# Kernel optimization log

Hardware: AMD Instinct MI355X
Metric: run time of the kernel (lower is better)

## Reference

```python
import jax, jax.numpy as jnp
import numpy as np

K_PLG = 9
LN_EPS = 1e-5

def _layer_norm(x, g, b):
    mu = jnp.mean(x, axis=-1, keepdims=True)
    v = jnp.mean((x - mu) ** 2, axis=-1, keepdims=True)
    return (x - mu) / jnp.sqrt(v + LN_EPS) * g + b

def _label_to_patch_agg(label, patch, k):
    # squared euclidean distances (S, N); sqrt is monotonic so top-k indices
    # match torch.cdist(p=2).topk(largest=False)
    d2 = (jnp.sum(label * label, axis=1)[:, None]
          + jnp.sum(patch * patch, axis=1)[None, :]
          - 2.0 * label @ patch.T)
    _, idx = jax.lax.top_k(-d2, k)          # (S, k) nearest
    nbr = patch[idx]                         # (S, k, C)
    return jnp.max(nbr - label[:, None, :], axis=1)  # max-relative diff (S, C)

def setup_inputs() -> dict:
    key = jax.random.key(0)
    ks = jax.random.split(key, 12)
    N, C = 100000, 256
    n_mood, n_genre, n_sub = 64, 256, 1024
    s = 1.0 / np.sqrt(C)
    return {
        "patch_emb": jax.random.normal(ks[0], (N, C), jnp.float32),
        "mood_emb": jax.random.normal(ks[1], (n_mood, C), jnp.float32),
        "genre_emb": jax.random.normal(ks[2], (n_genre, C), jnp.float32),
        "sub_emb": jax.random.normal(ks[3], (n_sub, C), jnp.float32),
        "Wm": jax.random.normal(ks[4], (2 * C, C), jnp.float32) * s,
        "bm": jnp.zeros((C,), jnp.float32),
        "Wg": jax.random.normal(ks[5], (3 * C, C), jnp.float32) * s,
        "bg": jnp.zeros((C,), jnp.float32),
        "Ws": jax.random.normal(ks[6], (4 * C, C), jnp.float32) * s,
        "bs": jnp.zeros((C,), jnp.float32),
        "gm": jnp.ones((C,), jnp.float32), "bnm": jnp.zeros((C,), jnp.float32),
        "gg": jnp.ones((C,), jnp.float32), "bng": jnp.zeros((C,), jnp.float32),
        "gs": jnp.ones((C,), jnp.float32), "bns": jnp.zeros((C,), jnp.float32),
    }

def reference(patch_emb, mood_emb, genre_emb, sub_emb,
              Wm, bm, Wg, bg, Ws, bs, gm, bnm, gg, bng, gs, bns):
    k = K_PLG
    # mood level
    ctx_m = _label_to_patch_agg(mood_emb, patch_emb, k)
    mood = _layer_norm(
        mood_emb + jnp.concatenate([mood_emb, ctx_m], axis=-1) @ Wm + bm, gm, bnm)
    # genre level
    ctx_g_p = _label_to_patch_agg(genre_emb, patch_emb, k)
    ctx_g_m = _label_to_patch_agg(genre_emb, mood, max(1, k // 2))
    genre = _layer_norm(
        genre_emb + jnp.concatenate([genre_emb, ctx_g_p, ctx_g_m], axis=-1) @ Wg + bg,
        gg, bng)
    # sub-genre level
    ctx_s_p = _label_to_patch_agg(sub_emb, patch_emb, k)
    ctx_s_m = _label_to_patch_agg(sub_emb, mood, max(1, k // 3))
    ctx_s_g = _label_to_patch_agg(sub_emb, genre, max(1, k // 2))
    sub = _layer_norm(
        sub_emb + jnp.concatenate([sub_emb, ctx_s_p, ctx_s_m, ctx_s_g], axis=-1) @ Ws + bs,
        gs, bns)
    return (mood, genre, sub)
```

## Files before the change

kernel.cpp:

```cpp
#include <hip/hip_runtime.h>
#include <float.h>

#define N_PATCH 100000
#define C 256
#define S_TOT 1344
#define LBLK 32
#define NGRP 42
#define NCHUNK 24
#define CHUNKP 4224
#define NTILE 1563
#define KCC 10
#define NCAND (NCHUNK*KCC)
#define NSEL 24
#define KP 9
#define SMASK 0xFFFFE000u
#define KINIT 0x7F7FFFFFu

typedef __attribute__((ext_vector_type(4))) float f32x4;
typedef __attribute__((ext_vector_type(2))) long i64x2;
typedef __attribute__((ext_vector_type(4))) unsigned int u32x4;

static __device__ __forceinline__ unsigned int pk4_fp8(float a, float b, float c, float d) {
  int v = __builtin_amdgcn_cvt_pk_fp8_f32(a, b, 0, false);
  v = __builtin_amdgcn_cvt_pk_fp8_f32(c, d, v, true);
  return (unsigned int)v;
}

#define KNET3(K0, K1, K2, KV)                               \
  { unsigned int _kv = (KV);                                \
    K2 = min(K2, max(K1, _kv));                             \
    K1 = min(K1, max(K0, _kv));                             \
    K0 = min(K0, _kv); }

__global__ __launch_bounds__(256) void k_prep(
    const float* __restrict__ patch, const float* __restrict__ me,
    const float* __restrict__ ge, const float* __restrict__ se,
    unsigned char* __restrict__ patchT, unsigned char* __restrict__ lblQ,
    float* __restrict__ hp2) {
  __shared__ float4 xs[4096];
  int bid = blockIdx.x;
  int t = threadIdx.x;
  if (bid < NTILE) {
    const int T = bid;
    const int w = t >> 6, l = t & 63;
    #pragma unroll
    for (int i = 0; i < 16; ++i) {
      int row = 4 * i + w;
      int grow = min(T * 64 + row, N_PATCH - 1);
      float4 v = reinterpret_cast<const float4*>(patch + (size_t)grow * C)[l];
      xs[row * 64 + (l ^ (row & 7))] = v;
      float s = v.x*v.x + v.y*v.y + v.z*v.z + v.w*v.w;
      #pragma unroll
      for (int off = 32; off; off >>= 1) s += __shfl_down(s, off, 64);
      if (l == 0 && T * 64 + row < N_PATCH) hp2[T * 64 + row] = 0.5f * s + 512.0f;
    }
    __syncthreads();
    const int q = (t >> 6) & 3, g = (t >> 4) & 3, r16 = t & 15;
    const int b4 = 16 * q + 2 * g;
    #pragma unroll
    for (int u = 0; u < 4; ++u) {
      int rr = u * 16 + r16;
      int xm = rr & 7;
      float4 aa = xs[rr * 64 + ((b4    ) ^ xm)];
      float4 bb = xs[rr * 64 + ((b4 + 1) ^ xm)];
      float4 cc = xs[rr * 64 + ((b4 + 8) ^ xm)];
      float4 dd = xs[rr * 64 + ((b4 + 9) ^ xm)];
      u32x4 o;
      o.x = pk4_fp8(-aa.x, -aa.y, -aa.z, -aa.w);
      o.y = pk4_fp8(-bb.x, -bb.y, -bb.z, -bb.w);
      o.z = pk4_fp8(-cc.x, -cc.y, -cc.z, -cc.w);
      o.w = pk4_fp8(-dd.x, -dd.y, -dd.z, -dd.w);
      *reinterpret_cast<u32x4*>(patchT + ((size_t)T << 14) + (size_t)(u * 256 + t) * 16) = o;
    }
  } else {
    int row = (bid - NTILE) * 4 + (t >> 6);
    int l = t & 63;
    int k0 = 32 * ((l >> 1) & 7) + 8 * (l >> 4) + (l & 1) * 4;
    const float* src = (row < 64) ? me + (size_t)row * C
                     : (row < 320) ? ge + (size_t)(row - 64) * C
                                   : se + (size_t)(row - 320) * C;
    float4 v = *reinterpret_cast<const float4*>(src + k0);
    *reinterpret_cast<unsigned int*>(lblQ + (size_t)row * 256 + l * 4) =
        pk4_fp8(v.x, v.y, v.z, v.w);
  }
}

__global__ __launch_bounds__(256, 4) void k_score_mfma(
    const unsigned char* __restrict__ patchT, const unsigned char* __restrict__ lblQ,
    const float* __restrict__ hp2,
    float* __restrict__ candS, int* __restrict__ candI) {
  __shared__ unsigned int ksmem[LBLK * 48];

  const int j = blockIdx.x;
  const int chunk = (j & 7) * 3 + (j >> 3) / NGRP;
  const int grp = (j >> 3) % NGRP;
  const int row0 = grp * LBLK;
  const int p_begin = chunk * CHUNKP;
  const int p_end = min(p_begin + CHUNKP, N_PATCH);
  const int tid = threadIdx.x;
  const int l = tid & 63, w = tid >> 6;
  const int g = l >> 4, r16 = l & 15;

  long bf0[8], bf1[8];
  {
    const unsigned char* b0 = lblQ + ((size_t)(row0 + r16) << 8) + (g << 6);
    #pragma unroll
    for (int q = 0; q < 4; ++q) {
      i64x2 v0 = *reinterpret_cast<const i64x2*>(b0 + q * 16);
      i64x2 v1 = *reinterpret_cast<const i64x2*>(b0 + 4096 + q * 16);
      bf0[2*q] = v0.x; bf0[2*q+1] = v0.y;
      bf1[2*q] = v1.x; bf1[2*q+1] = v1.y;
    }
  }

  unsigned int a0k = KINIT, a1k = KINIT, a2k = KINIT;
  unsigned int b0k = KINIT, b1k = KINIT, b2k = KINIT;

  const int nsteps = (p_end - p_begin + 63) >> 6;
  const int gtile0 = p_begin >> 6;
  const unsigned char* pbase = patchT + ((size_t)gtile0 << 14) + (w << 12) + (l << 4);
  const int hsub = w * 16 + 4 * g;

  i64x2 A0[4], A1[4];
  float4 h0, h1;

  auto loadA = [&](int t, i64x2 (&A)[4]) {
    const unsigned char* p = pbase + ((size_t)t << 14);
    #pragma unroll
    for (int q = 0; q < 4; ++q) A[q] = *reinterpret_cast<const i64x2*>(p + (q << 10));
  };
  auto loadH = [&](int t) -> float4 {
    int hi = p_begin + t * 64 + hsub;
    if (hi > N_PATCH - 4) hi = N_PATCH - 4;
    return *reinterpret_cast<const float4*>(hp2 + hi);
  };

  auto compute = [&](i64x2 (&A)[4], float4 h, int t) {
    f32x4 acc0 = {h.x, h.y, h.z, h.w};
    f32x4 acc1 = acc0;
    __builtin_amdgcn_s_setprio(1);
    #pragma unroll
    for (int q = 0; q < 4; ++q) {
      acc0 = __builtin_amdgcn_mfma_f32_16x16x32_fp8_fp8(A[q].x, bf0[2*q],   acc0, 0, 0, 0);
      acc1 = __builtin_amdgcn_mfma_f32_16x16x32_fp8_fp8(A[q].x, bf1[2*q],   acc1, 0, 0, 0);
      acc0 = __builtin_amdgcn_mfma_f32_16x16x32_fp8_fp8(A[q].y, bf0[2*q+1], acc0, 0, 0, 0);
      acc1 = __builtin_amdgcn_mfma_f32_16x16x32_fp8_fp8(A[q].y, bf1[2*q+1], acc1, 0, 0, 0);
    }
    __builtin_amdgcn_s_setprio(0);
    unsigned int lidx = (unsigned int)(t * 64 + hsub);
    unsigned int l1 = lidx | 1u, l2 = lidx | 2u, l3 = lidx | 3u;
    if (p_begin + t * 64 + 64 <= p_end) {
      KNET3(a0k, a1k, a2k, (__float_as_uint(acc0[0]) & SMASK) | lidx);
      KNET3(a0k, a1k, a2k, (__float_as_uint(acc0[1]) & SMASK) | l1);
      KNET3(a0k, a1k, a2k, (__float_as_uint(acc0[2]) & SMASK) | l2);
      KNET3(a0k, a1k, a2k, (__float_as_uint(acc0[3]) & SMASK) | l3);
      KNET3(b0k, b1k, b2k, (__float_as_uint(acc1[0]) & SMASK) | lidx);
      KNET3(b0k, b1k, b2k, (__float_as_uint(acc1[1]) & SMASK) | l1);
      KNET3(b0k, b1k, b2k, (__float_as_uint(acc1[2]) & SMASK) | l2);
      KNET3(b0k, b1k, b2k, (__float_as_uint(acc1[3]) & SMASK) | l3);
    } else {
      const int pg0 = p_begin + t * 64 + hsub;
      unsigned int k0 = (pg0     < p_end) ? ((__float_as_uint(acc0[0]) & SMASK) | lidx) : KINIT;
      unsigned int k1 = (pg0 + 1 < p_end) ? ((__float_as_uint(acc0[1]) & SMASK) | l1) : KINIT;
      unsigned int k2 = (pg0 + 2 < p_end) ? ((__float_as_uint(acc0[2]) & SMASK) | l2) : KINIT;
      unsigned int k3 = (pg0 + 3 < p_end) ? ((__float_as_uint(acc0[3]) & SMASK) | l3) : KINIT;
      unsigned int m0 = (pg0     < p_end) ? ((__float_as_uint(acc1[0]) & SMASK) | lidx) : KINIT;
      unsigned int m1 = (pg0 + 1 < p_end) ? ((__float_as_uint(acc1[1]) & SMASK) | l1) : KINIT;
      unsigned int m2 = (pg0 + 2 < p_end) ? ((__float_as_uint(acc1[2]) & SMASK) | l2) : KINIT;
      unsigned int m3 = (pg0 + 3 < p_end) ? ((__float_as_uint(acc1[3]) & SMASK) | l3) : KINIT;
      KNET3(a0k, a1k, a2k, k0); KNET3(a0k, a1k, a2k, k1);
      KNET3(a0k, a1k, a2k, k2); KNET3(a0k, a1k, a2k, k3);
      KNET3(b0k, b1k, b2k, m0); KNET3(b0k, b1k, b2k, m1);
      KNET3(b0k, b1k, b2k, m2); KNET3(b0k, b1k, b2k, m3);
    }
  };

  loadA(0, A0); h0 = loadH(0);
  for (int t = 0; t < nsteps; t += 2) {
    loadA(t + 1, A1); h1 = loadH(t + 1);
    compute(A0, h0, t);
    loadA(t + 2, A0); h0 = loadH(t + 2);
    if (t + 1 < nsteps) compute(A1, h1, t + 1);
  }
  __syncthreads();

  const int sub = (w << 2) + g;
  {
    int base0 = (r16 * 16 + sub) * 3;
    int base1 = ((r16 + 16) * 16 + sub) * 3;
    ksmem[base0 + 0] = a0k; ksmem[base0 + 1] = a1k; ksmem[base0 + 2] = a2k;
    ksmem[base1 + 0] = b0k; ksmem[base1 + 1] = b1k; ksmem[base1 + 2] = b2k;
  }
  __syncthreads();
  if (tid < LBLK) {
    unsigned int fk[KCC];
    #pragma unroll
    for (int jj = 0; jj < KCC; ++jj) fk[jj] = KINIT;
    for (int q = 0; q < 48; ++q) {
      unsigned int v = ksmem[tid * 48 + q];
      if (v < fk[KCC-1]) {
        fk[KCC-1] = v;
        #pragma unroll
        for (int qq = KCC-1; qq >= 1; --qq) {
          if (fk[qq] < fk[qq-1]) {
            unsigned int tv = fk[qq]; fk[qq] = fk[qq-1]; fk[qq-1] = tv;
          }
        }
      }
    }
    size_t o = ((size_t)(row0 + tid) * NCHUNK + chunk) * KCC;
    #pragma unroll
    for (int jj = 0; jj < KCC; ++jj) {
      candS[o + jj] = __uint_as_float(fk[jj] & SMASK);
      candI[o + jj] = p_begin + (int)(fk[jj] & 0x1FFFu);
    }
  }
}

__global__ __launch_bounds__(256) void k_rescore_ctx(
    const float* __restrict__ patchF,
    const float* __restrict__ me, const float* __restrict__ ge,
    const float* __restrict__ se,
    const float* __restrict__ hp2, const float* __restrict__ candS,
    const int* __restrict__ candI,
    float* __restrict__ ctx_m, float* __restrict__ ctx_gp, float* __restrict__ ctx_sp,
    const float* __restrict__ Wm, const float* __restrict__ bm,
    const float* __restrict__ gm, const float* __restrict__ bnm,
    float* __restrict__ out_m) {
  __shared__ float lrow[C];
  __shared__ float crow[C];
  __shared__ float ss[NCAND];
  __shared__ int si[NCAND];
  __shared__ int selIdx[NSEL];
  __shared__ float s2[NSEL];
  __shared__ int top[KP];
  __shared__ float red2[4];
  int row = blockIdx.x, t = threadIdx.x;
  const float* lsrc = (row < 64) ? me + (size_t)row * C
                    : (row < 320) ? ge + (size_t)(row - 64) * C
                                  : se + (size_t)(row - 320) * C;
  lrow[t] = lsrc[t];
  if (t < NCAND) {
    ss[t] = candS[(size_t)row * NCAND + t];
    si[t] = candI[(size_t)row * NCAND + t];
  }
  __syncthreads();
  if (t < NCAND) {
    float s = ss[t]; int id = si[t];
    int rank = 0;
    for (int q = 0; q < NCAND; ++q) {
      float v = ss[q];
      rank += (v < s) || (v == s && si[q] < id);
    }
    if (rank < NSEL) selIdx[rank] = id;
  }
  __syncthreads();
  {
    int c = t >> 3, l8 = t & 7;
    if (c < NSEL) {
      const float4* pr = reinterpret_cast<const float4*>(patchF + (size_t)selIdx[c] * C);
      const float4* lr = reinterpret_cast<const float4*>(lrow);
      float dx = 0.f, dy = 0.f, dz = 0.f, dw = 0.f;
      #pragma unroll
      for (int i = 0; i < 8; ++i) {
        float4 a = pr[l8 + 8*i], b = lr[l8 + 8*i];
        dx = fmaf(a.x, b.x, dx); dy = fmaf(a.y, b.y, dy);
        dz = fmaf(a.z, b.z, dz); dw = fmaf(a.w, b.w, dw);
      }
      float d = (dx + dy) + (dz + dw);
      #pragma unroll
      for (int off = 1; off < 8; off <<= 1) d += __shfl_xor(d, off, 64);
      if (l8 == 0) s2[c] = hp2[selIdx[c]] - d;
    }
  }
  __syncthreads();
  if (t == 0) {
    float fs[KP]; int fi[KP];
    #pragma unroll
    for (int jj = 0; jj < KP; ++jj) { fs[jj] = FLT_MAX; fi[jj] = 0; }
    for (int q = 0; q < NSEL; ++q) {
      float v = s2[q];
      if (v < fs[KP-1]) {
        fs[KP-1] = v; fi[KP-1] = selIdx[q];
        #pragma unroll
        for (int qq = KP-1; qq >= 1; --qq) {
          if (fs[qq] < fs[qq-1]) {
            float ts = fs[qq]; fs[qq] = fs[qq-1]; fs[qq-1] = ts;
            int ti = fi[qq]; fi[qq] = fi[qq-1]; fi[qq-1] = ti;
          }
        }
      }
    }
    #pragma unroll
    for (int jj = 0; jj < KP; ++jj) top[jj] = fi[jj];
  }
  __syncthreads();
  float m = -FLT_MAX;
  #pragma unroll
  for (int jj = 0; jj < KP; ++jj)
    m = fmaxf(m, patchF[(size_t)top[jj] * C + t]);
  float ctxv = m - lrow[t];
  float* dst; int rr;
  if (row < 64)       { dst = ctx_m;  rr = row; }
  else if (row < 320) { dst = ctx_gp; rr = row - 64; }
  else                { dst = ctx_sp; rr = row - 320; }
  dst[(size_t)rr * C + t] = ctxv;
  if (row < 64) {
    crow[t] = ctxv;
    __syncthreads();
    float acc = 0.f;
    for (int i0 = 0; i0 < 256; i0 += 16) {
      float wv[16];
      #pragma unroll
      for (int u = 0; u < 16; ++u) wv[u] = Wm[(size_t)(i0 + u) * C + t];
      #pragma unroll
      for (int u = 0; u < 16; ++u) acc = fmaf(lrow[i0 + u], wv[u], acc);
    }
    for (int i0 = 0; i0 < 256; i0 += 16) {
      float wv[16];
      #pragma unroll
      for (int u = 0; u < 16; ++u) wv[u] = Wm[(size_t)(256 + i0 + u) * C + t];
      #pragma unroll
      for (int u = 0; u < 16; ++u) acc = fmaf(crow[i0 + u], wv[u], acc);
    }
    float y = lrow[t] + acc + bm[t];
    int w = t >> 6, ln = t & 63;
    float sum = y;
    #pragma unroll
    for (int off = 32; off; off >>= 1) sum += __shfl_down(sum, off, 64);
    if (ln == 0) red2[w] = sum;
    __syncthreads();
    float mu = (red2[0] + red2[1] + red2[2] + red2[3]) * (1.f / C);
    __syncthreads();
    float d = y - mu;
    float sq = d * d;
    #pragma unroll
    for (int off = 32; off; off >>= 1) sq += __shfl_down(sq, off, 64);
    if (ln == 0) red2[w] = sq;
    __syncthreads();
    float var = (red2[0] + red2[1] + red2[2] + red2[3]) * (1.f / C);
    out_m[(size_t)row * C + t] = d * rsqrtf(var + 1e-5f) * gm[t] + bnm[t];
  }
}

__global__ __launch_bounds__(512) void k_out_g(
    const float* __restrict__ genre_e, const float* __restrict__ ctx_gp,
    const float* __restrict__ out_m,
    const float* __restrict__ W, const float* __restrict__ bias,
    const float* __restrict__ gamma, const float* __restrict__ beta,
    float* __restrict__ out) {
  __shared__ float x[2][1024];
  __shared__ float ds[2][64];
  __shared__ int sel[2][4];
  __shared__ float part[2][2][256];
  __shared__ float red[4][2];
  const int row0 = blockIdx.x * 2, t = threadIdx.x;
  const int w = t >> 6, ln = t & 63;
  if (t < 256) {
    int rr = t >> 7, seg = (t >> 6) & 1, c4 = (t & 63) << 2;
    const float* src = seg ? ctx_gp : genre_e;
    *reinterpret_cast<float4*>(&x[rr][seg * 256 + c4]) =
        *reinterpret_cast<const float4*>(src + (size_t)(row0 + rr) * C + c4);
  }
  __syncthreads();
  {
    int q = t & 3, pr = t >> 2;
    int rr = pr >> 6, ri = pr & 63;
    const float4* rp = reinterpret_cast<const float4*>(out_m + (size_t)ri * C);
    const float4* qp = reinterpret_cast<const float4*>(x[rr]);
    float s = 0.f;
    #pragma unroll
    for (int i = 0; i < 16; ++i) {
      float4 a = rp[i * 4 + q];
      float4 b = qp[i * 4 + q];
      float e;
      e = a.x - b.x; s = fmaf(e, e, s); e = a.y - b.y; s = fmaf(e, e, s);
      e = a.z - b.z; s = fmaf(e, e, s); e = a.w - b.w; s = fmaf(e, e, s);
    }
    s += __shfl_xor(s, 1, 64);
    s += __shfl_xor(s, 2, 64);
    if (q == 0) ds[rr][ri] = s;
  }
  __syncthreads();
  if (w < 2) {
    for (int jj = 0; jj < 4; ++jj) {
      float m = ds[w][ln]; int mi_ = ln;
      #pragma unroll
      for (int off = 32; off; off >>= 1) {
        float om = __shfl_down(m, off, 64);
        int oi = __shfl_down(mi_, off, 64);
        if (om < m) { m = om; mi_ = oi; }
      }
      mi_ = __shfl(mi_, 0, 64);
      if (ln == 0) sel[w][jj] = mi_;
      ds[w][mi_] = FLT_MAX;
    }
  }
  __syncthreads();
  {
    int rr = t >> 8, c = t & 255;
    float m = -FLT_MAX;
    #pragma unroll
    for (int jj = 0; jj < 4; ++jj) m = fmaxf(m, out_m[(size_t)sel[rr][jj] * C + c]);
    x[rr][512 + c] = m - x[rr][c];
  }
  __syncthreads();
  const int kg = t >> 8, col = t & 255, base = kg * 384;
  float a0 = 0.f, a1 = 0.f;
  for (int i0 = 0; i0 < 384; i0 += 16) {
    float wv[16];
    #pragma unroll
    for (int u = 0; u < 16; ++u) wv[u] = W[(size_t)(base + i0 + u) * C + col];
    #pragma unroll
    for (int u = 0; u < 16; ++u) {
      a0 = fmaf(x[0][base + i0 + u], wv[u], a0);
      a1 = fmaf(x[1][base + i0 + u], wv[u], a1);
    }
  }
  part[kg][0][col] = a0; part[kg][1][col] = a1;
  __syncthreads();
  if (t < 256) {
    float bv = bias[t];
    float y0 = x[0][t] + part[0][0][t] + part[1][0][t] + bv;
    float y1 = x[1][t] + part[0][1][t] + part[1][1][t] + bv;
    float s0 = y0, s1 = y1;
    #pragma unroll
    for (int off = 32; off; off >>= 1) {
      s0 += __shfl_down(s0, off, 64);
      s1 += __shfl_down(s1, off, 64);
    }
    if (ln == 0) { red[w][0] = s0; red[w][1] = s1; }
    __syncthreads();
    float mu0 = (red[0][0] + red[1][0] + red[2][0] + red[3][0]) * (1.f / C);
    float mu1 = (red[0][1] + red[1][1] + red[2][1] + red[3][1]) * (1.f / C);
    __syncthreads();
    float d0 = y0 - mu0, d1 = y1 - mu1;
    s0 = d0 * d0; s1 = d1 * d1;
    #pragma unroll
    for (int off = 32; off; off >>= 1) {
      s0 += __shfl_down(s0, off, 64);
      s1 += __shfl_down(s1, off, 64);
    }
    if (ln == 0) { red[w][0] = s0; red[w][1] = s1; }
    __syncthreads();
    float v0 = (red[0][0] + red[1][0] + red[2][0] + red[3][0]) * (1.f / C);
    float v1 = (red[0][1] + red[1][1] + red[2][1] + red[3][1]) * (1.f / C);
    float gv = gamma[t], bbv = beta[t];
    out[(size_t)(row0    ) * C + t] = d0 * rsqrtf(v0 + 1e-5f) * gv + bbv;
    out[(size_t)(row0 + 1) * C + t] = d1 * rsqrtf(v1 + 1e-5f) * gv + bbv;
  }
}

__global__ __launch_bounds__(512) void k_out_s(
    const float* __restrict__ sub_e, const float* __restrict__ ctx_sp,
    const float* __restrict__ out_m, const float* __restrict__ out_g,
    const float* __restrict__ W, const float* __restrict__ bias,
    const float* __restrict__ gamma, const float* __restrict__ beta,
    float* __restrict__ out) {
  __shared__ float x[4][1024];
  __shared__ float ds[4][256];
  __shared__ int sel[4][4];
  __shared__ float part[2][4][256];
  __shared__ float red[4][4];
  const int row0 = blockIdx.x * 4, t = threadIdx.x;
  const int w = t >> 6, ln = t & 63;
  {
    int rr = t >> 7, seg = (t >> 6) & 1, c4 = (t & 63) << 2;
    const float* src = seg ? ctx_sp : sub_e;
    *reinterpret_cast<float4*>(&x[rr][seg * 256 + c4]) =
        *reinterpret_cast<const float4*>(src + (size_t)(row0 + rr) * C + c4);
  }
  __syncthreads();
  #pragma unroll
  for (int u = 0; u < 2; ++u) {
    int unit = u * 512 + t;
    int q = unit & 3, pr = unit >> 2;
    int rr = pr >> 6, ri = pr & 63;
    const float4* rp = reinterpret_cast<const float4*>(out_m + (size_t)ri * C);
    const float4* qp = reinterpret_cast<const float4*>(x[rr]);
    float s = 0.f;
    #pragma unroll
    for (int i = 0; i < 16; ++i) {
      float4 a = rp[i * 4 + q];
      float4 b = qp[i * 4 + q];
      float e;
      e = a.x - b.x; s = fmaf(e, e, s); e = a.y - b.y; s = fmaf(e, e, s);
      e = a.z - b.z; s = fmaf(e, e, s); e = a.w - b.w; s = fmaf(e, e, s);
    }
    s += __shfl_xor(s, 1, 64);
    s += __shfl_xor(s, 2, 64);
    if (q == 0) ds[rr][ri] = s;
  }
  __syncthreads();
  if (w < 4) {
    for (int jj = 0; jj < 3; ++jj) {
      float m = ds[w][ln]; int mi_ = ln;
      #pragma unroll
      for (int off = 32; off; off >>= 1) {
        float om = __shfl_down(m, off, 64);
        int oi = __shfl_down(mi_, off, 64);
        if (om < m) { m = om; mi_ = oi; }
      }
      mi_ = __shfl(mi_, 0, 64);
      if (ln == 0) sel[w][jj] = mi_;
      ds[w][mi_] = FLT_MAX;
    }
  }
  __syncthreads();
  #pragma unroll
  for (int u = 0; u < 2; ++u) {
    int idx = u * 512 + t;
    int rr = idx >> 8, c = idx & 255;
    float m = -FLT_MAX;
    #pragma unroll
    for (int jj = 0; jj < 3; ++jj) m = fmaxf(m, out_m[(size_t)sel[rr][jj] * C + c]);
    x[rr][512 + c] = m - x[rr][c];
  }
  __syncthreads();
  #pragma unroll
  for (int u = 0; u < 8; ++u) {
    int unit = u * 512 + t;
    int q = unit & 3, pr = unit >> 2;
    int rr = pr >> 8, ri = pr & 255;
    const float4* rp = reinterpret_cast<const float4*>(out_g + (size_t)ri * C);
    const float4* qp = reinterpret_cast<const float4*>(x[rr]);
    float s = 0.f;
    #pragma unroll
    for (int i = 0; i < 16; ++i) {
      float4 a = rp[i * 4 + q];
      float4 b = qp[i * 4 + q];
      float e;
      e = a.x - b.x; s = fmaf(e, e, s); e = a.y - b.y; s = fmaf(e, e, s);
      e = a.z - b.z; s = fmaf(e, e, s); e = a.w - b.w; s = fmaf(e, e, s);
    }
    s += __shfl_xor(s, 1, 64);
    s += __shfl_xor(s, 2, 64);
    if (q == 0) ds[rr][ri] = s;
  }
  __syncthreads();
  if (w < 4) {
    for (int jj = 0; jj < 4; ++jj) {
      float m = ds[w][ln]; int mi_ = ln;
      #pragma unroll
      for (int o = 64; o < 256; o += 64) {
        float v = ds[w][ln + o];
        if (v < m) { m = v; mi_ = ln + o; }
      }
      #pragma unroll
      for (int off = 32; off; off >>= 1) {
        float om = __shfl_down(m, off, 64);
        int oi = __shfl_down(mi_, off, 64);
        if (om < m) { m = om; mi_ = oi; }
      }
      mi_ = __shfl(mi_, 0, 64);
      if (ln == 0) sel[w][jj] = mi_;
      ds[w][mi_] = FLT_MAX;
    }
  }
  __syncthreads();
  #pragma unroll
  for (int u = 0; u < 2; ++u) {
    int idx = u * 512 + t;
    int rr = idx >> 8, c = idx & 255;
    float m = -FLT_MAX;
    #pragma unroll
    for (int jj = 0; jj < 4; ++jj) m = fmaxf(m, out_g[(size_t)sel[rr][jj] * C + c]);
    x[rr][768 + c] = m - x[rr][c];
  }
  __syncthreads();
  const int kg = t >> 8, col = t & 255, base = kg * 512;
  float acc[4] = {0.f, 0.f, 0.f, 0.f};
  for (int i0 = 0; i0 < 512; i0 += 16) {
    float wv[16];
    #pragma unroll
    for (int u = 0; u < 16; ++u) wv[u] = W[(size_t)(base + i0 + u) * C + col];
    #pragma unroll
    for (int u = 0; u < 16; ++u) {
      #pragma unroll
      for (int rr = 0; rr < 4; ++rr) acc[rr] = fmaf(x[rr][base + i0 + u], wv[u], acc[rr]);
    }
  }
  #pragma unroll
  for (int rr = 0; rr < 4; ++rr) part[kg][rr][col] = acc[rr];
  __syncthreads();
  if (t < 256) {
    float bv = bias[t];
    float y[4], d[4];
    #pragma unroll
    for (int rr = 0; rr < 4; ++rr) {
      y[rr] = x[rr][t] + part[0][rr][t] + part[1][rr][t] + bv;
      float sum = y[rr];
      #pragma unroll
      for (int off = 32; off; off >>= 1) sum += __shfl_down(sum, off, 64);
      if (ln == 0) red[w][rr] = sum;
    }
    __syncthreads();
    float mu[4];
    #pragma unroll
    for (int rr = 0; rr < 4; ++rr)
      mu[rr] = (red[0][rr] + red[1][rr] + red[2][rr] + red[3][rr]) * (1.f / C);
    __syncthreads();
    #pragma unroll
    for (int rr = 0; rr < 4; ++rr) {
      d[rr] = y[rr] - mu[rr];
      float sq = d[rr] * d[rr];
      #pragma unroll
      for (int off = 32; off; off >>= 1) sq += __shfl_down(sq, off, 64);
      if (ln == 0) red[w][rr] = sq;
    }
    __syncthreads();
    #pragma unroll
    for (int rr = 0; rr < 4; ++rr) {
      float var = (red[0][rr] + red[1][rr] + red[2][rr] + red[3][rr]) * (1.f / C);
      out[(size_t)(row0 + rr) * C + t] = d[rr] * rsqrtf(var + 1e-5f) * gamma[t] + beta[t];
    }
  }
}

extern "C" void kernel_launch(void* const* d_in, const int* in_sizes, int n_in,
                              void* d_out, int out_size, void* d_ws, size_t ws_size,
                              hipStream_t stream) {
  const float* patch   = (const float*)d_in[0];
  const float* mood_e  = (const float*)d_in[1];
  const float* genre_e = (const float*)d_in[2];
  const float* sub_e   = (const float*)d_in[3];
  const float* Wm  = (const float*)d_in[4];
  const float* bm  = (const float*)d_in[5];
  const float* Wg  = (const float*)d_in[6];
  const float* bg  = (const float*)d_in[7];
  const float* Ws  = (const float*)d_in[8];
  const float* bs_ = (const float*)d_in[9];
  const float* gm  = (const float*)d_in[10];
  const float* bnm = (const float*)d_in[11];
  const float* gg  = (const float*)d_in[12];
  const float* bng = (const float*)d_in[13];
  const float* gs  = (const float*)d_in[14];
  const float* bns = (const float*)d_in[15];

  char* ws = (char*)d_ws;
  size_t off = 0;
  auto alloc = [&](size_t bytes) { void* p = ws + off; off = (off + bytes + 255) & ~(size_t)255; return p; };
  unsigned char* patchT = (unsigned char*)alloc((size_t)(NTILE + 2) * 16384);
  unsigned char* lblQ   = (unsigned char*)alloc((size_t)S_TOT * 256);
  float* hp2   = (float*)alloc((size_t)N_PATCH * 4);
  float* candS = (float*)alloc((size_t)S_TOT * NCAND * 4);
  int*   candI = (int*)  alloc((size_t)S_TOT * NCAND * 4);
  float* ctx_m  = (float*)alloc((size_t)64   * C * 4);
  float* ctx_gp = (float*)alloc((size_t)256  * C * 4);
  float* ctx_sp = (float*)alloc((size_t)1024 * C * 4);

  float* out_m = (float*)d_out;
  float* out_g = out_m + 64 * C;
  float* out_s = out_g + 256 * C;

  k_prep<<<NTILE + S_TOT / 4, 256, 0, stream>>>(patch, mood_e, genre_e, sub_e,
                                                patchT, lblQ, hp2);
  k_score_mfma<<<NGRP * NCHUNK, 256, 0, stream>>>(patchT, lblQ, hp2, candS, candI);
  k_rescore_ctx<<<S_TOT, 256, 0, stream>>>(patch, mood_e, genre_e, sub_e, hp2,
                                           candS, candI, ctx_m, ctx_gp, ctx_sp,
                                           Wm, bm, gm, bnm, out_m);
  k_out_g<<<128, 512, 0, stream>>>(genre_e, ctx_gp, out_m, Wg, bg, gg, bng, out_g);
  k_out_s<<<256, 512, 0, stream>>>(sub_e, ctx_sp, out_m, out_g, Ws, bs_, gs, bns, out_s);
}
```

Before: 186.4 us.

## Merge two label groups per score block so waves share patch tile loads

The scoring kernel now uses 512-thread blocks covering 64 labels instead of 256-thread blocks covering 32. The two halves of the block stream the same patch tiles, and per-step barriers keep them in lockstep so one half's loads can hit cache for the other. This is meant to cut redundant global/L2 traffic on the fp8 patch stream. In exchange it adds two barriers per loop iteration and halves the block count, which reduces occupancy flexibility.

```diff
diff --git a/kernel.cpp b/kernel.cpp
--- a/kernel.cpp
+++ b/kernel.cpp
@@ -4,8 +4,7 @@
 #define N_PATCH 100000
 #define C 256
 #define S_TOT 1344
-#define LBLK 32
-#define NGRP 42
+#define NPAIR 21
 #define NCHUNK 24
 #define CHUNKP 4224
 #define NTILE 1563
@@ -85,25 +84,27 @@
   }
 }
 
-__global__ __launch_bounds__(256, 4) void k_score_mfma(
+__global__ __launch_bounds__(512, 2) void k_score_mfma(
     const unsigned char* __restrict__ patchT, const unsigned char* __restrict__ lblQ,
     const float* __restrict__ hp2,
     float* __restrict__ candS, int* __restrict__ candI) {
-  __shared__ unsigned int ksmem[LBLK * 48];
+  __shared__ unsigned int ksmem[64 * 48];
 
   const int j = blockIdx.x;
-  const int chunk = (j & 7) * 3 + (j >> 3) / NGRP;
-  const int grp = (j >> 3) % NGRP;
-  const int row0 = grp * LBLK;
+  const int xcd = j & 7, r = j >> 3;
+  const int chunk = xcd * 3 + r / NPAIR;
+  const int pair = r % NPAIR;
+  const int row0 = pair * 64;
   const int p_begin = chunk * CHUNKP;
   const int p_end = min(p_begin + CHUNKP, N_PATCH);
   const int tid = threadIdx.x;
   const int l = tid & 63, w = tid >> 6;
+  const int wq = w & 3, half = w >> 2;
   const int g = l >> 4, r16 = l & 15;
 
   long bf0[8], bf1[8];
   {
-    const unsigned char* b0 = lblQ + ((size_t)(row0 + r16) << 8) + (g << 6);
+    const unsigned char* b0 = lblQ + ((size_t)(row0 + half * 32 + r16) << 8) + (g << 6);
     #pragma unroll
     for (int q = 0; q < 4; ++q) {
       i64x2 v0 = *reinterpret_cast<const i64x2*>(b0 + q * 16);
@@ -118,8 +119,8 @@
 
   const int nsteps = (p_end - p_begin + 63) >> 6;
   const int gtile0 = p_begin >> 6;
-  const unsigned char* pbase = patchT + ((size_t)gtile0 << 14) + (w << 12) + (l << 4);
-  const int hsub = w * 16 + 4 * g;
+  const unsigned char* pbase = patchT + ((size_t)gtile0 << 14) + (wq << 12) + (l << 4);
+  const int hsub = wq * 16 + 4 * g;
 
   i64x2 A0[4], A1[4];
   float4 h0, h1;
@@ -178,21 +179,24 @@
   loadA(0, A0); h0 = loadH(0);
   for (int t = 0; t < nsteps; t += 2) {
     loadA(t + 1, A1); h1 = loadH(t + 1);
+    __builtin_amdgcn_s_barrier();
     compute(A0, h0, t);
     loadA(t + 2, A0); h0 = loadH(t + 2);
+    __builtin_amdgcn_s_barrier();
     if (t + 1 < nsteps) compute(A1, h1, t + 1);
   }
   __syncthreads();
 
-  const int sub = (w << 2) + g;
+  const int sub = (wq << 2) + g;
+  const int labA = half * 32 + r16;
   {
-    int base0 = (r16 * 16 + sub) * 3;
-    int base1 = ((r16 + 16) * 16 + sub) * 3;
+    int base0 = (labA * 16 + sub) * 3;
+    int base1 = ((labA + 16) * 16 + sub) * 3;
     ksmem[base0 + 0] = a0k; ksmem[base0 + 1] = a1k; ksmem[base0 + 2] = a2k;
     ksmem[base1 + 0] = b0k; ksmem[base1 + 1] = b1k; ksmem[base1 + 2] = b2k;
   }
   __syncthreads();
-  if (tid < LBLK) {
+  if (tid < 64) {
     unsigned int fk[KCC];
     #pragma unroll
     for (int jj = 0; jj < KCC; ++jj) fk[jj] = KINIT;
@@ -655,7 +659,7 @@
 
   k_prep<<<NTILE + S_TOT / 4, 256, 0, stream>>>(patch, mood_e, genre_e, sub_e,
                                                 patchT, lblQ, hp2);
-  k_score_mfma<<<NGRP * NCHUNK, 256, 0, stream>>>(patchT, lblQ, hp2, candS, candI);
+  k_score_mfma<<<NPAIR * NCHUNK, 512, 0, stream>>>(patchT, lblQ, hp2, candS, candI);
   k_rescore_ctx<<<S_TOT, 256, 0, stream>>>(patch, mood_e, genre_e, sub_e, hp2,
                                            candS, candI, ctx_m, ctx_gp, ctx_sp,
                                            Wm, bm, gm, bnm, out_m);
```

Result: no change. 187.0 us (+0.3%).

## Switch scoring to 32x32x64 scaled FP8 MFMA with 128-patch tiles

Applied to the files above, without the earlier changes.

Replaces the 16x16x32 fp8 MFMA scoring loop with the gfx950 scaled 32x32x64 f8f6f4 MFMA, which cuts the instruction count per tile. Patch data is re-laid out in the prep kernel into 128-row tiles that match the new operand format, and label rows are now stored in plain order. Each lane keeps per-row top-3 lists in registers for 16 accumulator rows and merges them across half-waves with shuffles before the shared-memory reduction. The trade-offs are much higher register pressure (occupancy hint lowered from 4 to 3), a 4x larger final serial merge per label (192 entries instead of 48), and the loss of the previous double-buffered load prefetch.

```diff
diff --git a/kernel.cpp b/kernel.cpp
--- a/kernel.cpp
+++ b/kernel.cpp
@@ -8,16 +8,19 @@
 #define NGRP 42
 #define NCHUNK 24
 #define CHUNKP 4224
-#define NTILE 1563
+#define NTILE128 782
+#define NHALF 1564
 #define KCC 10
 #define NCAND (NCHUNK*KCC)
 #define NSEL 24
 #define KP 9
 #define SMASK 0xFFFFE000u
 #define KINIT 0x7F7FFFFFu
+#define SCL1 0x7F7F7F7Fu
 
 typedef __attribute__((ext_vector_type(4))) float f32x4;
-typedef __attribute__((ext_vector_type(2))) long i64x2;
+typedef __attribute__((ext_vector_type(16))) float f32x16;
+typedef __attribute__((ext_vector_type(8))) int v8i;
 typedef __attribute__((ext_vector_type(4))) unsigned int u32x4;
 
 static __device__ __forceinline__ unsigned int pk4_fp8(float a, float b, float c, float d) {
@@ -40,56 +43,59 @@
   __shared__ float4 xs[4096];
   int bid = blockIdx.x;
   int t = threadIdx.x;
-  if (bid < NTILE) {
-    const int T = bid;
+  if (bid < NHALF) {
+    const int T = bid >> 1, half = bid & 1;
+    const int rbase = T * 128 + half * 64;
     const int w = t >> 6, l = t & 63;
     #pragma unroll
     for (int i = 0; i < 16; ++i) {
       int row = 4 * i + w;
-      int grow = min(T * 64 + row, N_PATCH - 1);
+      int grow = min(rbase + row, N_PATCH - 1);
       float4 v = reinterpret_cast<const float4*>(patch + (size_t)grow * C)[l];
       xs[row * 64 + (l ^ (row & 7))] = v;
       float s = v.x*v.x + v.y*v.y + v.z*v.z + v.w*v.w;
       #pragma unroll
       for (int off = 32; off; off >>= 1) s += __shfl_down(s, off, 64);
-      if (l == 0 && T * 64 + row < N_PATCH) hp2[T * 64 + row] = 0.5f * s + 512.0f;
-    }
-    __syncthreads();
-    const int q = (t >> 6) & 3, g = (t >> 4) & 3, r16 = t & 15;
-    const int b4 = 16 * q + 2 * g;
-    #pragma unroll
-    for (int u = 0; u < 4; ++u) {
-      int rr = u * 16 + r16;
-      int xm = rr & 7;
-      float4 aa = xs[rr * 64 + ((b4    ) ^ xm)];
-      float4 bb = xs[rr * 64 + ((b4 + 1) ^ xm)];
-      float4 cc = xs[rr * 64 + ((b4 + 8) ^ xm)];
-      float4 dd = xs[rr * 64 + ((b4 + 9) ^ xm)];
+      if (l == 0 && rbase + row < N_PATCH) hp2[rbase + row] = 0.5f * s + 512.0f;
+    }
+    __syncthreads();
+    #pragma unroll
+    for (int it = 0; it < 4; ++it) {
+      int c = it * 256 + t;
+      int w_rel = c >> 9, q = (c >> 7) & 3, part = (c >> 6) & 1, ll = c & 63;
+      int row = w_rel * 32 + (ll & 31);
+      int k4 = (q * 64 + (ll >> 5) * 32 + part * 16) >> 2;
+      int xm = row & 7;
+      float4 f0 = xs[row * 64 + ((k4 + 0) ^ xm)];
+      float4 f1 = xs[row * 64 + ((k4 + 1) ^ xm)];
+      float4 f2 = xs[row * 64 + ((k4 + 2) ^ xm)];
+      float4 f3 = xs[row * 64 + ((k4 + 3) ^ xm)];
       u32x4 o;
-      o.x = pk4_fp8(-aa.x, -aa.y, -aa.z, -aa.w);
-      o.y = pk4_fp8(-bb.x, -bb.y, -bb.z, -bb.w);
-      o.z = pk4_fp8(-cc.x, -cc.y, -cc.z, -cc.w);
-      o.w = pk4_fp8(-dd.x, -dd.y, -dd.z, -dd.w);
-      *reinterpret_cast<u32x4*>(patchT + ((size_t)T << 14) + (size_t)(u * 256 + t) * 16) = o;
+      o.x = pk4_fp8(-f0.x, -f0.y, -f0.z, -f0.w);
+      o.y = pk4_fp8(-f1.x, -f1.y, -f1.z, -f1.w);
+      o.z = pk4_fp8(-f2.x, -f2.y, -f2.z, -f2.w);
+      o.w = pk4_fp8(-f3.x, -f3.y, -f3.z, -f3.w);
+      size_t dst = (size_t)T * 32768 + (size_t)(half * 2 + w_rel) * 8192
+                 + q * 2048 + part * 1024 + ll * 16;
+      *reinterpret_cast<u32x4*>(patchT + dst) = o;
     }
   } else {
-    int row = (bid - NTILE) * 4 + (t >> 6);
+    int row = (bid - NHALF) * 4 + (t >> 6);
     int l = t & 63;
-    int k0 = 32 * ((l >> 1) & 7) + 8 * (l >> 4) + (l & 1) * 4;
     const float* src = (row < 64) ? me + (size_t)row * C
                      : (row < 320) ? ge + (size_t)(row - 64) * C
                                    : se + (size_t)(row - 320) * C;
-    float4 v = *reinterpret_cast<const float4*>(src + k0);
+    float4 v = *reinterpret_cast<const float4*>(src + 4 * l);
     *reinterpret_cast<unsigned int*>(lblQ + (size_t)row * 256 + l * 4) =
         pk4_fp8(v.x, v.y, v.z, v.w);
   }
 }
 
-__global__ __launch_bounds__(256, 4) void k_score_mfma(
+__global__ __launch_bounds__(256, 3) void k_score_mfma(
     const unsigned char* __restrict__ patchT, const unsigned char* __restrict__ lblQ,
     const float* __restrict__ hp2,
     float* __restrict__ candS, int* __restrict__ candI) {
-  __shared__ unsigned int ksmem[LBLK * 48];
+  __shared__ unsigned int ksmem[LBLK * 192];
 
   const int j = blockIdx.x;
   const int chunk = (j & 7) * 3 + (j >> 3) / NGRP;
@@ -99,105 +105,83 @@
   const int p_end = min(p_begin + CHUNKP, N_PATCH);
   const int tid = threadIdx.x;
   const int l = tid & 63, w = tid >> 6;
-  const int g = l >> 4, r16 = l & 15;
-
-  long bf0[8], bf1[8];
+  const int lh = l >> 5, l31 = l & 31;
+
+  v8i A[4];
   {
-    const unsigned char* b0 = lblQ + ((size_t)(row0 + r16) << 8) + (g << 6);
+    const unsigned char* lb = lblQ + ((size_t)(row0 + l31)) * 256 + lh * 32;
     #pragma unroll
     for (int q = 0; q < 4; ++q) {
-      i64x2 v0 = *reinterpret_cast<const i64x2*>(b0 + q * 16);
-      i64x2 v1 = *reinterpret_cast<const i64x2*>(b0 + 4096 + q * 16);
-      bf0[2*q] = v0.x; bf0[2*q+1] = v0.y;
-      bf1[2*q] = v1.x; bf1[2*q+1] = v1.y;
-    }
-  }
-
-  unsigned int a0k = KINIT, a1k = KINIT, a2k = KINIT;
-  unsigned int b0k = KINIT, b1k = KINIT, b2k = KINIT;
-
-  const int nsteps = (p_end - p_begin + 63) >> 6;
-  const int gtile0 = p_begin >> 6;
-  const unsigned char* pbase = patchT + ((size_t)gtile0 << 14) + (w << 12) + (l << 4);
-  const int hsub = w * 16 + 4 * g;
-
-  i64x2 A0[4], A1[4];
-  float4 h0, h1;
-
-  auto loadA = [&](int t, i64x2 (&A)[4]) {
-    const unsigned char* p = pbase + ((size_t)t << 14);
-    #pragma unroll
-    for (int q = 0; q < 4; ++q) A[q] = *reinterpret_cast<const i64x2*>(p + (q << 10));
-  };
-  auto loadH = [&](int t) -> float4 {
-    int hi = p_begin + t * 64 + hsub;
-    if (hi > N_PATCH - 4) hi = N_PATCH - 4;
-    return *reinterpret_cast<const float4*>(hp2 + hi);
-  };
-
-  auto compute = [&](i64x2 (&A)[4], float4 h, int t) {
-    f32x4 acc0 = {h.x, h.y, h.z, h.w};
-    f32x4 acc1 = acc0;
+      u32x4 lo = *reinterpret_cast<const u32x4*>(lb + q * 64);
+      u32x4 hi = *reinterpret_cast<const u32x4*>(lb + q * 64 + 16);
+      A[q] = v8i{(int)lo.x, (int)lo.y, (int)lo.z, (int)lo.w,
+                 (int)hi.x, (int)hi.y, (int)hi.z, (int)hi.w};
+    }
+  }
+
+  unsigned int kk0[16], kk1[16], kk2[16];
+  #pragma unroll
+  for (int r = 0; r < 16; ++r) { kk0[r] = KINIT; kk1[r] = KINIT; kk2[r] = KINIT; }
+
+  const int nsteps = (p_end - p_begin + 127) >> 7;
+  const unsigned char* pb = patchT + ((size_t)(p_begin >> 7)) * 32768 + (w << 13) + (l << 4);
+  const int ploc = w * 32 + l31;
+
+  for (int t = 0; t < nsteps; ++t) {
+    const unsigned char* pt = pb + (size_t)t * 32768;
+    v8i B[4];
+    #pragma unroll
+    for (int q = 0; q < 4; ++q) {
+      u32x4 lo = *reinterpret_cast<const u32x4*>(pt + (q << 11));
+      u32x4 hi = *reinterpret_cast<const u32x4*>(pt + (q << 11) + 1024);
+      B[q] = v8i{(int)lo.x, (int)lo.y, (int)lo.z, (int)lo.w,
+                 (int)hi.x, (int)hi.y, (int)hi.z, (int)hi.w};
+    }
+    const int p = p_begin + t * 128 + ploc;
+    const float h = hp2[min(p, N_PATCH - 1)];
+    f32x16 acc;
+    #pragma unroll
+    for (int i = 0; i < 16; ++i) acc[i] = h;
     __builtin_amdgcn_s_setprio(1);
     #pragma unroll
-    for (int q = 0; q < 4; ++q) {
-      acc0 = __builtin_amdgcn_mfma_f32_16x16x32_fp8_fp8(A[q].x, bf0[2*q],   acc0, 0, 0, 0);
-      acc1 = __builtin_amdgcn_mfma_f32_16x16x32_fp8_fp8(A[q].x, bf1[2*q],   acc1, 0, 0, 0);
-      acc0 = __builtin_amdgcn_mfma_f32_16x16x32_fp8_fp8(A[q].y, bf0[2*q+1], acc0, 0, 0, 0);
-      acc1 = __builtin_amdgcn_mfma_f32_16x16x32_fp8_fp8(A[q].y, bf1[2*q+1], acc1, 0, 0, 0);
-    }
+    for (int q = 0; q < 4; ++q)
+      acc = __builtin_amdgcn_mfma_scale_f32_32x32x64_f8f6f4(
+          A[q], B[q], acc, 0, 0, 0, SCL1, 0, SCL1);
     __builtin_amdgcn_s_setprio(0);
-    unsigned int lidx = (unsigned int)(t * 64 + hsub);
-    unsigned int l1 = lidx | 1u, l2 = lidx | 2u, l3 = lidx | 3u;
-    if (p_begin + t * 64 + 64 <= p_end) {
-      KNET3(a0k, a1k, a2k, (__float_as_uint(acc0[0]) & SMASK) | lidx);
-      KNET3(a0k, a1k, a2k, (__float_as_uint(acc0[1]) & SMASK) | l1);
-      KNET3(a0k, a1k, a2k, (__float_as_uint(acc0[2]) & SMASK) | l2);
-      KNET3(a0k, a1k, a2k, (__float_as_uint(acc0[3]) & SMASK) | l3);
-      KNET3(b0k, b1k, b2k, (__float_as_uint(acc1[0]) & SMASK) | lidx);
-      KNET3(b0k, b1k, b2k, (__float_as_uint(acc1[1]) & SMASK) | l1);
-      KNET3(b0k, b1k, b2k, (__float_as_uint(acc1[2]) & SMASK) | l2);
-      KNET3(b0k, b1k, b2k, (__float_as_uint(acc1[3]) & SMASK) | l3);
-    } else {
-      const int pg0 = p_begin + t * 64 + hsub;
-      unsigned int k0 = (pg0     < p_end) ? ((__float_as_uint(acc0[0]) & SMASK) | lidx) : KINIT;
-      unsigned int k1 = (pg0 + 1 < p_end) ? ((__float_as_uint(acc0[1]) & SMASK) | l1) : KINIT;
-      unsigned int k2 = (pg0 + 2 < p_end) ? ((__float_as_uint(acc0[2]) & SMASK) | l2) : KINIT;
-      unsigned int k3 = (pg0 + 3 < p_end) ? ((__float_as_uint(acc0[3]) & SMASK) | l3) : KINIT;
-      unsigned int m0 = (pg0     < p_end) ? ((__float_as_uint(acc1[0]) & SMASK) | lidx) : KINIT;
-      unsigned int m1 = (pg0 + 1 < p_end) ? ((__float_as_uint(acc1[1]) & SMASK) | l1) : KINIT;
-      unsigned int m2 = (pg0 + 2 < p_end) ? ((__float_as_uint(acc1[2]) & SMASK) | l2) : KINIT;
-      unsigned int m3 = (pg0 + 3 < p_end) ? ((__float_as_uint(acc1[3]) & SMASK) | l3) : KINIT;
-      KNET3(a0k, a1k, a2k, k0); KNET3(a0k, a1k, a2k, k1);
-      KNET3(a0k, a1k, a2k, k2); KNET3(a0k, a1k, a2k, k3);
-      KNET3(b0k, b1k, b2k, m0); KNET3(b0k, b1k, b2k, m1);
-      KNET3(b0k, b1k, b2k, m2); KNET3(b0k, b1k, b2k, m3);
-    }
-  };
-
-  loadA(0, A0); h0 = loadH(0);
-  for (int t = 0; t < nsteps; t += 2) {
-    loadA(t + 1, A1); h1 = loadH(t + 1);
-    compute(A0, h0, t);
-    loadA(t + 2, A0); h0 = loadH(t + 2);
-    if (t + 1 < nsteps) compute(A1, h1, t + 1);
-  }
-  __syncthreads();
-
-  const int sub = (w << 2) + g;
-  {
-    int base0 = (r16 * 16 + sub) * 3;
-    int base1 = ((r16 + 16) * 16 + sub) * 3;
-    ksmem[base0 + 0] = a0k; ksmem[base0 + 1] = a1k; ksmem[base0 + 2] = a2k;
-    ksmem[base1 + 0] = b0k; ksmem[base1 + 1] = b1k; ksmem[base1 + 2] = b2k;
+    if (p < p_end) {
+      const unsigned int pidx = (unsigned int)(t * 128 + ploc);
+      #pragma unroll
+      for (int r = 0; r < 16; ++r)
+        KNET3(kk0[r], kk1[r], kk2[r], (__float_as_uint(acc[r]) & SMASK) | pidx);
+    }
+  }
+
+  #pragma unroll
+  for (int r = 0; r < 16; ++r) {
+    unsigned int o0 = __shfl_xor(kk0[r], 16, 64);
+    unsigned int o1 = __shfl_xor(kk1[r], 16, 64);
+    unsigned int o2 = __shfl_xor(kk2[r], 16, 64);
+    unsigned int m0 = min(kk0[r], o0);
+    unsigned int m1 = min(max(kk0[r], o0), min(kk1[r], o1));
+    unsigned int m2 = min(min(max(kk1[r], o0), max(o1, kk0[r])), min(kk2[r], o2));
+    kk0[r] = m0; kk1[r] = m1; kk2[r] = m2;
+  }
+  if ((l & 16) == 0) {
+    int g = l & 15;
+    #pragma unroll
+    for (int r = 0; r < 16; ++r) {
+      int L = (r & 3) + 8 * (r >> 2) + 4 * lh;
+      int base = L * 192 + w * 48 + g * 3;
+      ksmem[base] = kk0[r]; ksmem[base + 1] = kk1[r]; ksmem[base + 2] = kk2[r];
+    }
   }
   __syncthreads();
   if (tid < LBLK) {
     unsigned int fk[KCC];
     #pragma unroll
     for (int jj = 0; jj < KCC; ++jj) fk[jj] = KINIT;
-    for (int q = 0; q < 48; ++q) {
-      unsigned int v = ksmem[tid * 48 + q];
+    for (int q = 0; q < 192; ++q) {
+      unsigned int v = ksmem[tid * 192 + q];
       if (v < fk[KCC-1]) {
         fk[KCC-1] = v;
         #pragma unroll
@@ -640,7 +624,7 @@
   char* ws = (char*)d_ws;
   size_t off = 0;
   auto alloc = [&](size_t bytes) { void* p = ws + off; off = (off + bytes + 255) & ~(size_t)255; return p; };
-  unsigned char* patchT = (unsigned char*)alloc((size_t)(NTILE + 2) * 16384);
+  unsigned char* patchT = (unsigned char*)alloc((size_t)(NTILE128 + 2) * 32768);
   unsigned char* lblQ   = (unsigned char*)alloc((size_t)S_TOT * 256);
   float* hp2   = (float*)alloc((size_t)N_PATCH * 4);
   float* candS = (float*)alloc((size_t)S_TOT * NCAND * 4);
@@ -653,7 +637,7 @@
   float* out_g = out_m + 64 * C;
   float* out_s = out_g + 256 * C;
 
-  k_prep<<<NTILE + S_TOT / 4, 256, 0, stream>>>(patch, mood_e, genre_e, sub_e,
+  k_prep<<<NHALF + S_TOT / 4, 256, 0, stream>>>(patch, mood_e, genre_e, sub_e,
                                                 patchT, lblQ, hp2);
   k_score_mfma<<<NGRP * NCHUNK, 256, 0, stream>>>(patchT, lblQ, hp2, candS, candI);
   k_rescore_ctx<<<S_TOT, 256, 0, stream>>>(patch, mood_e, genre_e, sub_e, hp2,
```

After: 205.8 us. 10.4% more time.
